# Performance work log

Measured on AMD Instinct MI355X. Metric: run time of the kernel, lower is better.

Reference implementation:

```python
import jax, jax.numpy as jnp
import numpy as np

BS = 128
E4M3_MAX = 448.0
E5M2_MAX = 57344.0


def qdq(x, fmax, dt):
    # block-wise (128-wide, last dim) fp8 quantize + dequantize (simulates act_quant + dequant in fp8_gemm)
    *lead, K = x.shape
    xb = x.reshape(*lead, K // BS, BS)
    s = jnp.maximum(jnp.max(jnp.abs(xb), axis=-1, keepdims=True) / fmax, 1e-12)
    xq = (xb / s).astype(dt).astype(jnp.float32)
    return (xq * s).reshape(*lead, K)


def fp8_linear(x, w, w_scale, fmax, dt, bias=None):
    # weight is fp8-valued (stored as f32 of the rounded values) with per-output-row-block scales
    x_dq = qdq(x, fmax, dt)
    sv = jnp.repeat(w_scale, BS)[: w.shape[0]]
    y = jnp.einsum('btk,ok->bto', x_dq, w * sv[:, None])
    return y if bias is None else y + bias


def fp8_ln(x, g, gs, b, bsc, eps=1e-5):
    mean = jnp.mean(x, axis=-1, keepdims=True)
    var = jnp.mean(jnp.square(x - mean), axis=-1, keepdims=True)  # unbiased=False
    xn = (x - mean) / jnp.sqrt(var + eps)
    d = x.shape[-1]
    return xn * (g * jnp.repeat(gs, BS)[:d]) + (b * jnp.repeat(bsc, BS)[:d])


def _fwd(x, attn_mask, wq, qs, wk, ks, wv, vs, wo, os_, fc1_w, fc1_s, fc1_b, fc2_w, fc2_s, fc2_b,
         ln1_g, ln1_gs, ln1_b, ln1_bs, ln2_g, ln2_gs, ln2_b, ln2_bs):
    B, T, C = x.shape
    H = 16
    HD = C // H
    e5 = jnp.float8_e5m2
    # attention (q/k/v/out projections use E5M2 fp8)
    q = fp8_linear(x, wq, qs, E5M2_MAX, e5).reshape(B, T, H, HD).transpose(0, 2, 1, 3)
    k = fp8_linear(x, wk, ks, E5M2_MAX, e5).reshape(B, T, H, HD).transpose(0, 2, 1, 3)
    v = fp8_linear(x, wv, vs, E5M2_MAX, e5).reshape(B, T, H, HD).transpose(0, 2, 1, 3)
    scores = jnp.einsum('bhqd,bhkd->bhqk', q, k) / jnp.sqrt(jnp.float32(HD))
    scores = jnp.where(attn_mask[:, None] == 0, -jnp.inf, scores)
    attn = jax.nn.softmax(scores, axis=-1)  # dropout = identity (eval)
    ctx = jnp.einsum('bhqk,bhkd->bhqd', attn, v).transpose(0, 2, 1, 3).reshape(B, T, C)
    attn_out = fp8_linear(ctx, wo, os_, E5M2_MAX, e5)
    x = fp8_ln(x + attn_out, ln1_g, ln1_gs, ln1_b, ln1_bs)
    # MLP (E4M3 fp8)
    e4 = jnp.float8_e4m3fn
    h = fp8_linear(x, fc1_w, fc1_s, E4M3_MAX, e4, fc1_b)
    h = jax.nn.gelu(h, approximate=False)  # torch nn.GELU default = exact erf
    ffn = fp8_linear(h, fc2_w, fc2_s, E4M3_MAX, e4, fc2_b)
    x = fp8_ln(x + ffn, ln2_g, ln2_gs, ln2_b, ln2_bs)
    return x


def _xavier_fp8(key, out_f, in_f, dt):
    bound = float(np.sqrt(6.0 / (in_f + out_f)))
    w = jax.random.uniform(key, (out_f, in_f), jnp.float32, -bound, bound)
    return w.astype(dt).astype(jnp.float32)  # simulate fp8 storage


def setup_inputs() -> dict:
    key = jax.random.key(0)
    kk = jax.random.split(key, 8)
    B, T, C, MLP = 2, 1024, 2048, 8192
    e5, e4 = jnp.float8_e5m2, jnp.float8_e4m3fn
    x = jax.random.normal(kk[0], (B, T, C), jnp.float32)
    attn_mask = jnp.broadcast_to(jnp.tril(jnp.ones((T, T), jnp.int32))[None], (B, T, T))
    nb = C // BS  # 16
    inp = {
        'x': x,
        'attn_mask': attn_mask,
        'wq': _xavier_fp8(kk[1], C, C, e5), 'qs': jnp.ones(nb, jnp.float32),
        'wk': _xavier_fp8(kk[2], C, C, e5), 'ks': jnp.ones(nb, jnp.float32),
        'wv': _xavier_fp8(kk[3], C, C, e5), 'vs': jnp.ones(nb, jnp.float32),
        'wo': _xavier_fp8(kk[4], C, C, e5), 'os_': jnp.ones(nb, jnp.float32),
        'fc1_w': _xavier_fp8(kk[5], MLP, C, e4), 'fc1_s': jnp.ones(MLP // BS, jnp.float32), 'fc1_b': jnp.zeros(MLP, jnp.float32),
        'fc2_w': _xavier_fp8(kk[6], C, MLP, e4), 'fc2_s': jnp.ones(nb, jnp.float32), 'fc2_b': jnp.zeros(C, jnp.float32),
        'ln1_g': jnp.ones(C, jnp.float32), 'ln1_gs': jnp.ones(nb, jnp.float32),
        'ln1_b': jnp.zeros(C, jnp.float32), 'ln1_bs': jnp.ones(nb, jnp.float32),
        'ln2_g': jnp.ones(C, jnp.float32), 'ln2_gs': jnp.ones(nb, jnp.float32),
        'ln2_b': jnp.zeros(C, jnp.float32), 'ln2_bs': jnp.ones(nb, jnp.float32),
    }
    return inp


def reference(x, attn_mask, wq, qs, wk, ks, wv, vs, wo, os_, fc1_w, fc1_s, fc1_b, fc2_w, fc2_s, fc2_b,
              ln1_g, ln1_gs, ln1_b, ln1_bs, ln2_g, ln2_gs, ln2_b, ln2_bs):
    return _fwd(x, attn_mask, wq, qs, wk, ks, wv, vs, wo, os_, fc1_w, fc1_s, fc1_b, fc2_w, fc2_s, fc2_b,
                ln1_g, ln1_gs, ln1_b, ln1_bs, ln2_g, ln2_gs, ln2_b, ln2_bs)
```

## Files before the change

kernel.cpp:

```cpp
#include <hip/hip_runtime.h>
#include <cstdint>


typedef __bf16 bf16x8 __attribute__((ext_vector_type(8)));
typedef unsigned short u16x8 __attribute__((ext_vector_type(8)));
typedef float f32x4 __attribute__((ext_vector_type(4)));
typedef float f32x16 __attribute__((ext_vector_type(16)));
typedef int i32x8 __attribute__((ext_vector_type(8)));
typedef unsigned short u16;

#if __has_builtin(__builtin_amdgcn_exp2f)
#define EXP2F(x) __builtin_amdgcn_exp2f(x)
#else
#define EXP2F(x) exp2f(x)
#endif

__device__ __forceinline__ void gl_lds16(const void* g, void* l) {
  __builtin_amdgcn_global_load_lds(
      (const __attribute__((address_space(1))) void*)g,
      (__attribute__((address_space(3))) void*)l, 16, 0, 0);
}

struct u4x2 { uint4 a, b; };
__device__ __forceinline__ i32x8 pack8(uint4 lo, uint4 hi) {
  u4x2 t{lo, hi};
  return __builtin_bit_cast(i32x8, t);
}

__device__ __forceinline__ u16 bf16_rne(float v) {
  uint32_t u = __float_as_uint(v);
  u += 0x7FFFu + ((u >> 16) & 1u);
  return (u16)(u >> 16);
}

__device__ __forceinline__ float fp8_round(float v, int mbits, float minnorm, float subq) {
  float av = fabsf(v);
  if (av < minnorm) {
    return rintf(v / subq) * subq;
  }
  uint32_t u = __float_as_uint(v);
  const int shift = 23 - mbits;
  const uint32_t mask = (1u << shift) - 1u;
  const uint32_t rem = u & mask;
  uint32_t base = u & ~mask;
  const uint32_t half = 1u << (shift - 1);
  if (rem > half || (rem == half && ((base >> shift) & 1u))) base += (1u << shift);
  return __uint_as_float(base);
}

__device__ __forceinline__ uint8_t fp8_encode(float v, int mbits, int bias) {
  uint32_t u = __float_as_uint(v);
  uint32_t sign = (u >> 31) << 7;
  if ((u & 0x7FFFFFFFu) == 0) return (uint8_t)sign;
  int e = (int)((u >> 23) & 255u) - 127;
  if (e >= 1 - bias) {
    uint32_t mant = (u >> (23 - mbits)) & ((1u << mbits) - 1u);
    return (uint8_t)(sign | ((uint32_t)(e + bias) << mbits) | mant);
  }
  float q = fabsf(v) * __uint_as_float((uint32_t)(127 + bias - 1 + mbits) << 23);
  return (uint8_t)(sign | (uint32_t)q);
}

__device__ __forceinline__ uint8_t q_e5(float v, float sc) {
  return fp8_encode(fp8_round(v / sc, 2, 6.103515625e-05f, 1.52587890625e-05f), 2, 15);
}
__device__ __forceinline__ uint8_t q_e4(float v, float sc) {
  return fp8_encode(fp8_round(v / sc, 3, 0.015625f, 0.001953125f), 3, 7);
}

__global__ __launch_bounds__(256) void qdq_kernel(
    const float* __restrict__ x, uint8_t* __restrict__ q, float* __restrict__ sT,
    int nblk, int kbshift, float fmax, float minnorm, float subq, int mbits, int bias) {
  const int wid = blockIdx.x * 4 + (threadIdx.x >> 6);
  if (wid >= nblk) return;
  const int lane = threadIdx.x & 63;
  const size_t base = (size_t)wid * 128 + (size_t)lane * 2;
  float2 v = *(const float2*)(x + base);
  float am = fmaxf(fabsf(v.x), fabsf(v.y));
#pragma unroll
  for (int m = 32; m >= 1; m >>= 1) am = fmaxf(am, __shfl_xor(am, m));
  const float sc = fmaxf(am / fmax, 1e-12f);
  const float q0 = fp8_round(v.x / sc, mbits, minnorm, subq);
  const float q1 = fp8_round(v.y / sc, mbits, minnorm, subq);
  uchar2 o;
  o.x = fp8_encode(q0, mbits, bias);
  o.y = fp8_encode(q1, mbits, bias);
  *(uchar2*)(q + base) = o;
  if (lane == 0) {
    const int kbs = 1 << kbshift;
    const int m = wid >> kbshift;
    const int kb = wid & (kbs - 1);
    sT[(size_t)kb * (nblk >> kbshift) + m] = sc;
  }
}

__global__ __launch_bounds__(256) void w_to_fp8_kernel(
    const float* __restrict__ in, uint8_t* __restrict__ out, int n4, int mbits, int bias) {
  const int i = blockIdx.x * 256 + threadIdx.x;
  if (i >= n4) return;
  float4 v = ((const float4*)in)[i];
  uchar4 o;
  o.x = fp8_encode(v.x, mbits, bias);
  o.y = fp8_encode(v.y, mbits, bias);
  o.z = fp8_encode(v.z, mbits, bias);
  o.w = fp8_encode(v.w, mbits, bias);
  *(uchar4*)(out + (size_t)i * 4) = o;
}

__global__ __launch_bounds__(256) void w3_to_fp8_kernel(
    const float* __restrict__ a, const float* __restrict__ b,
    const float* __restrict__ c, uint8_t* __restrict__ out, int n4) {
  const int i = blockIdx.x * 256 + threadIdx.x;
  if (i >= n4) return;
  const float* in = blockIdx.y == 0 ? a : (blockIdx.y == 1 ? b : c);
  float4 v = ((const float4*)in)[i];
  uchar4 o;
  o.x = fp8_encode(v.x, 2, 15);
  o.y = fp8_encode(v.y, 2, 15);
  o.z = fp8_encode(v.z, 2, 15);
  o.w = fp8_encode(v.w, 2, 15);
  *(uchar4*)(out + (size_t)blockIdx.y * n4 * 4 + (size_t)i * 4) = o;
}

__global__ void concat3_kernel(const float* __restrict__ a, const float* __restrict__ b,
                               const float* __restrict__ c, float* __restrict__ o, int n) {
  const int i = threadIdx.x;
  if (i < n) { o[i] = a[i]; o[n + i] = b[i]; o[2 * n + i] = c[i]; }
}

__global__ __launch_bounds__(256) void split_bf16_kernel(
    const float* __restrict__ in, u16* __restrict__ hi, u16* __restrict__ lo, int n4) {
  const int i = blockIdx.x * 256 + threadIdx.x;
  if (i >= n4) return;
  float4 v = ((const float4*)in)[i];
  float f[4] = {v.x, v.y, v.z, v.w};
  ushort4 oh, ol;
  u16* ph = (u16*)&oh;
  u16* pl = (u16*)&ol;
#pragma unroll
  for (int j = 0; j < 4; ++j) {
    u16 h = bf16_rne(f[j]);
    float hf = __uint_as_float((uint32_t)h << 16);
    ph[j] = h;
    pl[j] = bf16_rne(f[j] - hf);
  }
  ((ushort4*)hi)[i] = oh;
  ((ushort4*)lo)[i] = ol;
}

__global__ __launch_bounds__(256) void vtrans_kernel(
    const float* __restrict__ v, u16* __restrict__ vth, u16* __restrict__ vtl) {
  __shared__ float tile[64][65];
  const int tid = threadIdx.x;
  const int t0 = blockIdx.x * 64;
  const int d0 = blockIdx.y * 64;
  const int bh = blockIdx.z;
  const int b = bh >> 4, h = bh & 15;
#pragma unroll
  for (int s = 0; s < 4; ++s) {
    const int e = s * 256 + tid;
    const int r = e >> 4, c4 = e & 15;
    float4 val = *(const float4*)(v + ((size_t)(b * 1024 + t0 + r)) * 2048 + h * 128 + d0 + c4 * 4);
    tile[r][c4 * 4 + 0] = val.x;
    tile[r][c4 * 4 + 1] = val.y;
    tile[r][c4 * 4 + 2] = val.z;
    tile[r][c4 * 4 + 3] = val.w;
  }
  __syncthreads();
#pragma unroll
  for (int s = 0; s < 4; ++s) {
    const int e = s * 256 + tid;
    const int dr = e >> 4, tc4 = e & 15;
    ushort4 oh, ol;
    u16* ph = (u16*)&oh;
    u16* pl = (u16*)&ol;
#pragma unroll
    for (int i = 0; i < 4; ++i) {
      float f = tile[tc4 * 4 + i][dr];
      u16 hv = bf16_rne(f);
      ph[i] = hv;
      pl[i] = bf16_rne(f - __uint_as_float((uint32_t)hv << 16));
    }
    const size_t ob = ((size_t)(bh * 128 + d0 + dr)) * 1024 + t0 + tc4 * 4;
    *(ushort4*)(vth + ob) = oh;
    *(ushort4*)(vtl + ob) = ol;
  }
}

__global__ __launch_bounds__(256, 2) void attn_wave_kernel(
    const float* __restrict__ Q, const u16* __restrict__ Kh, const u16* __restrict__ Kl,
    const u16* __restrict__ Vth, const u16* __restrict__ Vtl,
    uint8_t* __restrict__ Aqo, float* __restrict__ sTo) {
  constexpr int PLD = 34;
  __shared__ uint32_t Psm[4][32 * PLD];
  __shared__ float Osum[32 * 128];
  __shared__ float lsh[4][32];

  const int tid = threadIdx.x;
  const int w = tid >> 6;
  const int lane = tid & 63;
  const int l31 = lane & 31;
  const int q2 = lane >> 5;
  const int bh = blockIdx.x;
  const int b = bh >> 4;
  const int hofs = (bh & 15) * 128;
  const int qt = 31 - (int)blockIdx.y;
  const int i0 = qt * 32;
  const float SC2 = 0.12752698f;

  bf16x8 qh[8], ql[8];
  {
    const float* qp = Q + ((size_t)(b * 1024 + i0 + l31)) * 2048 + hofs + q2 * 8;
#pragma unroll
    for (int c = 0; c < 8; ++c) {
      float4 v0 = *(const float4*)(qp + c * 16);
      float4 v1 = *(const float4*)(qp + c * 16 + 4);
      float f[8] = {v0.x, v0.y, v0.z, v0.w, v1.x, v1.y, v1.z, v1.w};
      u16x8 uh, ul;
#pragma unroll
      for (int j = 0; j < 8; ++j) {
        u16 hv = bf16_rne(f[j]);
        uh[j] = hv;
        ul[j] = bf16_rne(f[j] - __uint_as_float((uint32_t)hv << 16));
      }
      qh[c] = __builtin_bit_cast(bf16x8, uh);
      ql[c] = __builtin_bit_cast(bf16x8, ul);
    }
  }

  const f32x16 z16 = {0.f};
  f32x16 Oacc[4] = {z16, z16, z16, z16};
  float lr[16];
#pragma unroll
  for (int r = 0; r < 16; ++r) lr[r] = 0.f;
  int rowq[16];
#pragma unroll
  for (int r = 0; r < 16; ++r) rowq[r] = (r & 3) + 8 * (r >> 2) + 4 * q2;

  uint32_t* Pw = Psm[w];
  for (int kt = w; kt <= qt; kt += 4) {
    const int j0 = kt * 32;
    const size_t krow = ((size_t)(b * 1024 + j0 + l31)) * 2048 + hofs + q2 * 8;
    f32x16 S = z16;
#pragma unroll
    for (int c = 0; c < 8; ++c) {
      bf16x8 k8h = *(const bf16x8*)(Kh + krow + c * 16);
      bf16x8 k8l = *(const bf16x8*)(Kl + krow + c * 16);
      __builtin_amdgcn_s_setprio(1);
      S = __builtin_amdgcn_mfma_f32_32x32x16_bf16(qh[c], k8h, S, 0, 0, 0);
      S = __builtin_amdgcn_mfma_f32_32x32x16_bf16(qh[c], k8l, S, 0, 0, 0);
      S = __builtin_amdgcn_mfma_f32_32x32x16_bf16(ql[c], k8h, S, 0, 0, 0);
      __builtin_amdgcn_s_setprio(0);
    }
    if (kt == qt) {
#pragma unroll
      for (int r = 0; r < 16; ++r)
        if (l31 > rowq[r]) S[r] = -3e38f;
    }
#pragma unroll
    for (int r = 0; r < 16; ++r) {
      const float p = EXP2F(S[r] * SC2);
      lr[r] += p;
      const u16 ph = bf16_rne(p);
      const u16 pl = bf16_rne(p - __uint_as_float((uint32_t)ph << 16));
      Pw[rowq[r] * PLD + l31] = (uint32_t)ph | ((uint32_t)pl << 16);
    }
#pragma unroll
    for (int s = 0; s < 2; ++s) {
      const uint32_t* rp = Pw + l31 * PLD + s * 16 + q2 * 8;
      uint2 a0 = *(const uint2*)(rp + 0);
      uint2 a1 = *(const uint2*)(rp + 2);
      uint2 a2 = *(const uint2*)(rp + 4);
      uint2 a3 = *(const uint2*)(rp + 6);
      u16x8 uh, ul;
      uh[0] = (u16)a0.x; ul[0] = (u16)(a0.x >> 16);
      uh[1] = (u16)a0.y; ul[1] = (u16)(a0.y >> 16);
      uh[2] = (u16)a1.x; ul[2] = (u16)(a1.x >> 16);
      uh[3] = (u16)a1.y; ul[3] = (u16)(a1.y >> 16);
      uh[4] = (u16)a2.x; ul[4] = (u16)(a2.x >> 16);
      uh[5] = (u16)a2.y; ul[5] = (u16)(a2.y >> 16);
      uh[6] = (u16)a3.x; ul[6] = (u16)(a3.x >> 16);
      uh[7] = (u16)a3.y; ul[7] = (u16)(a3.y >> 16);
      bf16x8 p8h = __builtin_bit_cast(bf16x8, uh);
      bf16x8 p8l = __builtin_bit_cast(bf16x8, ul);
      const size_t vrow = ((size_t)(bh * 128 + l31)) * 1024 + j0 + s * 16 + q2 * 8;
#pragma unroll
      for (int dt = 0; dt < 4; ++dt) {
        bf16x8 v8h = *(const bf16x8*)(Vth + vrow + (size_t)dt * 32768);
        bf16x8 v8l = *(const bf16x8*)(Vtl + vrow + (size_t)dt * 32768);
        __builtin_amdgcn_s_setprio(1);
        Oacc[dt] = __builtin_amdgcn_mfma_f32_32x32x16_bf16(p8h, v8h, Oacc[dt], 0, 0, 0);
        Oacc[dt] = __builtin_amdgcn_mfma_f32_32x32x16_bf16(p8h, v8l, Oacc[dt], 0, 0, 0);
        Oacc[dt] = __builtin_amdgcn_mfma_f32_32x32x16_bf16(p8l, v8h, Oacc[dt], 0, 0, 0);
        __builtin_amdgcn_s_setprio(0);
      }
    }
  }

#pragma unroll
  for (int r = 0; r < 16; ++r) {
    float t = lr[r];
    t += __shfl_xor(t, 1);
    t += __shfl_xor(t, 2);
    t += __shfl_xor(t, 4);
    t += __shfl_xor(t, 8);
    t += __shfl_xor(t, 16);
    lr[r] = t;
  }
  if (l31 == 0) {
#pragma unroll
    for (int r = 0; r < 16; ++r) lsh[w][rowq[r]] = lr[r];
  }
  if (w == 0) {
#pragma unroll
    for (int dt = 0; dt < 4; ++dt)
#pragma unroll
      for (int r = 0; r < 16; ++r) Osum[rowq[r] * 128 + dt * 32 + l31] = Oacc[dt][r];
  }
  __syncthreads();
  if (w == 1) {
#pragma unroll
    for (int dt = 0; dt < 4; ++dt)
#pragma unroll
      for (int r = 0; r < 16; ++r) Osum[rowq[r] * 128 + dt * 32 + l31] += Oacc[dt][r];
  }
  __syncthreads();
  if (w == 2) {
#pragma unroll
    for (int dt = 0; dt < 4; ++dt)
#pragma unroll
      for (int r = 0; r < 16; ++r) Osum[rowq[r] * 128 + dt * 32 + l31] += Oacc[dt][r];
  }
  __syncthreads();
  if (w == 3) {
#pragma unroll
    for (int dt = 0; dt < 4; ++dt)
#pragma unroll
      for (int r = 0; r < 16; ++r) Osum[rowq[r] * 128 + dt * 32 + l31] += Oacc[dt][r];
  }
  __syncthreads();
  const int row = w * 8 + (lane >> 3);
  const int c0 = (lane & 7) * 16;
  const float inv = 1.0f / (lsh[0][row] + lsh[1][row] + lsh[2][row] + lsh[3][row]);
  float vq[16];
  float am = 0.f;
#pragma unroll
  for (int i2 = 0; i2 < 4; ++i2) {
    float4 v = *(const float4*)(Osum + row * 128 + c0 + i2 * 4);
    vq[i2 * 4 + 0] = v.x * inv;
    vq[i2 * 4 + 1] = v.y * inv;
    vq[i2 * 4 + 2] = v.z * inv;
    vq[i2 * 4 + 3] = v.w * inv;
  }
#pragma unroll
  for (int t = 0; t < 16; ++t) am = fmaxf(am, fabsf(vq[t]));
  am = fmaxf(am, __shfl_xor(am, 1));
  am = fmaxf(am, __shfl_xor(am, 2));
  am = fmaxf(am, __shfl_xor(am, 4));
  const float sc = fmaxf(am / 57344.f, 1e-12f);
  uint8_t qb8[16];
#pragma unroll
  for (int t = 0; t < 16; ++t) qb8[t] = q_e5(vq[t], sc);
  const int token = b * 1024 + i0 + row;
  *(uint4*)(Aqo + (size_t)token * 2048 + hofs + c0) = *(const uint4*)qb8;
  if ((lane & 7) == 0) sTo[(size_t)(bh & 15) * 2048 + token] = sc;
}

template <int FMT, int QOUT>
__global__ __launch_bounds__(256, 2) void gemm_simple(
    const uint8_t* __restrict__ A, const float* __restrict__ sxT,
    const uint8_t* __restrict__ W, const float* __restrict__ wsc,
    const float* __restrict__ bias, float* __restrict__ out,
    uint8_t* __restrict__ outq, float* __restrict__ sTq,
    int M, int N, int K, int gelu, int seg_shift, int Nw) {
  __shared__ uint8_t As[128 * 128];
  __shared__ uint8_t Ws[128 * 128];
  __shared__ float rowred[2][128];
  const int tid = threadIdx.x;
  const int lane = tid & 63;
  const int wave = tid >> 6;
  const int wm = (wave >> 1) * 64;
  const int wn = (wave & 1) * 64;
  const int l31 = lane & 31;
  const int q2 = lane >> 5;
  const int bm = blockIdx.y * 128;
  const int bn = blockIdx.x * 128;

  const int srow = wave * 8 + (lane >> 3);
  const int gchunk = (lane & 7) ^ (lane >> 3);
  const uint8_t* ga = A + (size_t)(bm + srow) * K + gchunk * 16;
  const uint8_t* gw = W + (size_t)(bn + srow) * K + gchunk * 16;
  uint8_t* la = As + srow * 128 + (lane & 7) * 16;
  uint8_t* lw = Ws + srow * 128 + (lane & 7) * 16;

  const f32x16 z16 = {0.f};
  f32x16 acc[2][2] = {{z16, z16}, {z16, z16}};

  const int nk = K >> 7;
  for (int kt = 0; kt < nk; ++kt) {
    __syncthreads();
#pragma unroll
    for (int s = 0; s < 4; ++s) {
      gl_lds16(ga + (size_t)s * 32 * K, la + s * 4096);
      gl_lds16(gw + (size_t)s * 32 * K, lw + s * 4096);
    }
    ga += 128;
    gw += 128;
    __syncthreads();
    f32x16 chk[2][2] = {{z16, z16}, {z16, z16}};
#pragma unroll
    for (int mf = 0; mf < 2; ++mf) {
      i32x8 af[2], bf2[2];
      const int c = mf * 4 + q2 * 2;
#pragma unroll
      for (int i = 0; i < 2; ++i) {
        const int r = wm + i * 32 + l31;
        const uint8_t* Ar = As + r * 128;
        const int s7 = r & 7;
        af[i] = pack8(*(const uint4*)(Ar + ((c ^ s7) * 16)),
                      *(const uint4*)(Ar + (((c + 1) ^ s7) * 16)));
      }
#pragma unroll
      for (int j = 0; j < 2; ++j) {
        const int r = wn + j * 32 + l31;
        const uint8_t* Wr = Ws + r * 128;
        const int s7 = r & 7;
        bf2[j] = pack8(*(const uint4*)(Wr + ((c ^ s7) * 16)),
                       *(const uint4*)(Wr + (((c + 1) ^ s7) * 16)));
      }
#pragma unroll
      for (int i = 0; i < 2; ++i)
#pragma unroll
        for (int j = 0; j < 2; ++j)
          chk[i][j] = __builtin_amdgcn_mfma_scale_f32_32x32x64_f8f6f4(
              af[i], bf2[j], chk[i][j], FMT, FMT, 0, 0x7F7F7F7F, 0, 0x7F7F7F7F);
    }
#pragma unroll
    for (int i = 0; i < 2; ++i) {
#pragma unroll
      for (int rg = 0; rg < 4; ++rg) {
        const f32x4 sv = *(const f32x4*)(sxT + (size_t)kt * M + bm + wm + i * 32 + rg * 8 + q2 * 4);
#pragma unroll
        for (int j = 0; j < 2; ++j)
#pragma unroll
          for (int rr = 0; rr < 4; ++rr)
            acc[i][j][rg * 4 + rr] += sv[rr] * chk[i][j][rg * 4 + rr];
      }
    }
  }

  if (QOUT) {
#pragma unroll
    for (int i = 0; i < 2; ++i) {
#pragma unroll
      for (int j = 0; j < 2; ++j) {
        const int n = bn + wn + j * 32 + l31;
        const float wsn = wsc[n >> 7];
        const float bv = bias[n];
#pragma unroll
        for (int reg = 0; reg < 16; ++reg) {
          float v = acc[i][j][reg] * wsn + bv;
          acc[i][j][reg] = 0.5f * v * (1.f + erff(v * 0.70710678118654752440f));
        }
      }
    }
#pragma unroll
    for (int i = 0; i < 2; ++i) {
      float am2[16];
#pragma unroll
      for (int reg = 0; reg < 16; ++reg)
        am2[reg] = fmaxf(fabsf(acc[i][0][reg]), fabsf(acc[i][1][reg]));
#pragma unroll
      for (int reg = 0; reg < 16; ++reg) {
        am2[reg] = fmaxf(am2[reg], __shfl_xor(am2[reg], 1));
        am2[reg] = fmaxf(am2[reg], __shfl_xor(am2[reg], 2));
        am2[reg] = fmaxf(am2[reg], __shfl_xor(am2[reg], 4));
        am2[reg] = fmaxf(am2[reg], __shfl_xor(am2[reg], 8));
        am2[reg] = fmaxf(am2[reg], __shfl_xor(am2[reg], 16));
      }
      if (l31 == 0) {
#pragma unroll
        for (int reg = 0; reg < 16; ++reg)
          rowred[wave & 1][wm + i * 32 + (reg & 3) + 8 * (reg >> 2) + 4 * q2] = am2[reg];
      }
    }
    __syncthreads();
#pragma unroll
    for (int i = 0; i < 2; ++i) {
#pragma unroll
      for (int reg = 0; reg < 16; ++reg) {
        const int rloc = wm + i * 32 + (reg & 3) + 8 * (reg >> 2) + 4 * q2;
        const float sc = fmaxf(fmaxf(rowred[0][rloc], rowred[1][rloc]) / 448.f, 1e-12f);
        const int m = bm + rloc;
#pragma unroll
        for (int j = 0; j < 2; ++j)
          outq[(size_t)m * N + bn + wn + j * 32 + l31] = q_e4(acc[i][j][reg], sc);
        if ((wave & 1) == 0 && l31 == 0) sTq[(size_t)(bn >> 7) * M + m] = sc;
      }
    }
    return;
  }

#pragma unroll
  for (int i = 0; i < 2; ++i) {
#pragma unroll
    for (int j = 0; j < 2; ++j) {
      const int n = bn + wn + j * 32 + l31;
      const float wsn = wsc[n >> 7];
      const float bv = bias ? bias[n] : 0.f;
      const int seg = n >> seg_shift;
      const int col = n & ((1 << seg_shift) - 1);
      float* op = out + (size_t)seg * M * Nw + col;
#pragma unroll
      for (int reg = 0; reg < 16; ++reg) {
        const int m = bm + wm + i * 32 + (reg & 3) + 8 * (reg >> 2) + 4 * q2;
        float v = acc[i][j][reg] * wsn + bv;
        if (gelu) v = 0.5f * v * (1.f + erff(v * 0.70710678118654752440f));
        op[(size_t)m * Nw] = v;
      }
    }
  }
}

template <int QOUT>
__global__ __launch_bounds__(256) void ln_kernel(
    const float* __restrict__ a, const float* __restrict__ b2,
    const float* __restrict__ g, const float* __restrict__ gs,
    const float* __restrict__ bb, const float* __restrict__ bs,
    float* __restrict__ out, uint8_t* __restrict__ outq, float* __restrict__ sT,
    int C) {
  __shared__ float red[4];
  __shared__ float wred[8][4];
  const int tid = threadIdx.x;
  const int row = blockIdx.x;
  const float* pa = a + (size_t)row * C;
  const float* pb = b2 + (size_t)row * C;
  float v[8];
  float sum = 0.f;
#pragma unroll
  for (int k = 0; k < 8; ++k) {
    const int c = tid + (k << 8);
    v[k] = pa[c] + pb[c];
    sum += v[k];
  }
#pragma unroll
  for (int m = 32; m >= 1; m >>= 1) sum += __shfl_xor(sum, m);
  if ((tid & 63) == 0) red[tid >> 6] = sum;
  __syncthreads();
  const float mean = (red[0] + red[1] + red[2] + red[3]) * (1.f / 2048.f);
  __syncthreads();
  float sq = 0.f;
#pragma unroll
  for (int k = 0; k < 8; ++k) {
    const float d = v[k] - mean;
    sq += d * d;
  }
#pragma unroll
  for (int m = 32; m >= 1; m >>= 1) sq += __shfl_xor(sq, m);
  if ((tid & 63) == 0) red[tid >> 6] = sq;
  __syncthreads();
  const float var = (red[0] + red[1] + red[2] + red[3]) * (1.f / 2048.f);
  const float inv = 1.0f / sqrtf(var + 1e-5f);
  float* po = out + (size_t)row * C;
  float o[8];
#pragma unroll
  for (int k = 0; k < 8; ++k) {
    const int c = tid + (k << 8);
    o[k] = (v[k] - mean) * inv * (g[c] * gs[c >> 7]) + bb[c] * bs[c >> 7];
    po[c] = o[k];
  }
  if (QOUT) {
    const int w = tid >> 6;
#pragma unroll
    for (int k = 0; k < 8; ++k) {
      float am = fabsf(o[k]);
      am = fmaxf(am, __shfl_xor(am, 1));
      am = fmaxf(am, __shfl_xor(am, 2));
      am = fmaxf(am, __shfl_xor(am, 4));
      am = fmaxf(am, __shfl_xor(am, 8));
      am = fmaxf(am, __shfl_xor(am, 16));
      am = fmaxf(am, __shfl_xor(am, 32));
      if ((tid & 63) == 0) wred[k][w] = am;
    }
    __syncthreads();
    const int hsel = (tid >> 7) * 2;
#pragma unroll
    for (int k = 0; k < 8; ++k) {
      const float bm = fmaxf(wred[k][hsel], wred[k][hsel + 1]);
      const float sc = fmaxf(bm / 448.f, 1e-12f);
      const int c = tid + (k << 8);
      outq[(size_t)row * C + c] = q_e4(o[k], sc);
      if ((tid & 127) == 0) sT[(size_t)((k << 1) | (tid >> 7)) * 2048 + row] = sc;
    }
  }
}

extern "C" void kernel_launch(void* const* d_in, const int* in_sizes, int n_in,
                              void* d_out, int out_size, void* d_ws, size_t ws_size,
                              hipStream_t stream) {
  const int C = 2048, MLP = 8192;
  const int M = 2048;

  const float* x = (const float*)d_in[0];
  const float* wq = (const float*)d_in[2];
  const float* qs = (const float*)d_in[3];
  const float* wk = (const float*)d_in[4];
  const float* ks = (const float*)d_in[5];
  const float* wv = (const float*)d_in[6];
  const float* vs = (const float*)d_in[7];
  const float* wo = (const float*)d_in[8];
  const float* os_ = (const float*)d_in[9];
  const float* fc1_w = (const float*)d_in[10];
  const float* fc1_s = (const float*)d_in[11];
  const float* fc1_b = (const float*)d_in[12];
  const float* fc2_w = (const float*)d_in[13];
  const float* fc2_s = (const float*)d_in[14];
  const float* fc2_b = (const float*)d_in[15];
  const float* ln1_g = (const float*)d_in[16];
  const float* ln1_gs = (const float*)d_in[17];
  const float* ln1_b = (const float*)d_in[18];
  const float* ln1_bs = (const float*)d_in[19];
  const float* ln2_g = (const float*)d_in[20];
  const float* ln2_gs = (const float*)d_in[21];
  const float* ln2_b = (const float*)d_in[22];
  const float* ln2_bs = (const float*)d_in[23];

  char* ws = (char*)d_ws;
  const size_t o_Aq = 0;
  const size_t o_Wb = 33554432;
  const size_t o_sx = 67108864;
  const size_t o_ln1 = 67633152;
  const size_t o_q = 84410368;
  const size_t o_k = 101187584;
  const size_t o_v = 117964800;
  const size_t o_ctx = 134742016;
  const size_t o_attn = 151519232;
  const size_t o_ffn = o_attn;
  if (ws_size < 168296448ull) return;

  uint8_t* Aq = (uint8_t*)(ws + o_Aq);
  uint8_t* Wb = (uint8_t*)(ws + o_Wb);
  float* sx = (float*)(ws + o_sx);
  float* wsc3 = (float*)(ws + o_sx + 262144);
  float* ln1o = (float*)(ws + o_ln1);
  float* qb = (float*)(ws + o_q);
  float* kb = (float*)(ws + o_k);
  float* vb = (float*)(ws + o_v);
  uint8_t* Aq2 = (uint8_t*)(ws + o_ctx);
  float* attn_out = (float*)(ws + o_attn);
  uint8_t* Aq3 = (uint8_t*)(ws + o_q);
  float* sxk = (float*)(ws + o_k);
  float* ffn = (float*)(ws + o_ffn);
  float* outp = (float*)d_out;
  u16* Kh = (u16*)(ws + o_Aq);
  u16* Kl = (u16*)(ws + o_Aq + 8388608);
  u16* Vth = (u16*)(ws + o_Aq + 16777216);
  u16* Vtl = (u16*)(ws + o_Aq + 25165824);

  const float E5_MAX = 57344.f, E5_MINN = 6.103515625e-05f, E5_SUBQ = 1.52587890625e-05f;
  const float E4_MAX = 448.f, E4_MINN = 0.015625f, E4_SUBQ = 0.001953125f;

  const dim3 blk(256);
  const int wc_qkv = (C * C / 4 + 255) / 256;
  const int wc_fc = (C * MLP / 4 + 255) / 256;

  qdq_kernel<<<M * (C / 128) / 4, blk, 0, stream>>>(x, Aq, sx, M * (C / 128), 4, E5_MAX, E5_MINN, E5_SUBQ, 2, 15);
  w3_to_fp8_kernel<<<dim3(wc_qkv, 3), blk, 0, stream>>>(wq, wk, wv, Wb, C * C / 4);
  concat3_kernel<<<1, 64, 0, stream>>>(qs, ks, vs, wsc3, C / 128);
  gemm_simple<1, 0><<<dim3(3 * C / 128, M / 128), blk, 0, stream>>>(
      Aq, sx, Wb, wsc3, nullptr, qb, nullptr, nullptr, M, 3 * C, C, 0, 11, C);

  split_bf16_kernel<<<(M * C / 4 + 255) / 256, blk, 0, stream>>>(kb, Kh, Kl, M * C / 4);
  vtrans_kernel<<<dim3(16, 2, 32), blk, 0, stream>>>(vb, Vth, Vtl);
  attn_wave_kernel<<<dim3(32, 32), blk, 0, stream>>>(qb, Kh, Kl, Vth, Vtl, Aq2, sx);

  w_to_fp8_kernel<<<wc_qkv, blk, 0, stream>>>(wo, Wb, C * C / 4, 2, 15);
  gemm_simple<1, 0><<<dim3(C / 128, M / 128), blk, 0, stream>>>(
      Aq2, sx, Wb, os_, nullptr, attn_out, nullptr, nullptr, M, C, C, 0, 30, C);

  ln_kernel<1><<<M, blk, 0, stream>>>(x, attn_out, ln1_g, ln1_gs, ln1_b, ln1_bs,
                                      ln1o, Aq, sx, C);

  w_to_fp8_kernel<<<wc_fc, blk, 0, stream>>>(fc1_w, Wb, C * MLP / 4, 3, 7);
  gemm_simple<0, 1><<<dim3(MLP / 128, M / 128), blk, 0, stream>>>(
      Aq, sx, Wb, fc1_s, fc1_b, nullptr, Aq3, sxk, M, MLP, C, 1, 30, MLP);

  w_to_fp8_kernel<<<wc_fc, blk, 0, stream>>>(fc2_w, Wb, C * MLP / 4, 3, 7);
  gemm_simple<0, 0><<<dim3(C / 128, M / 128), blk, 0, stream>>>(
      Aq3, sxk, Wb, fc2_s, fc2_b, ffn, nullptr, nullptr, M, C, MLP, 0, 30, C);

  ln_kernel<0><<<M, blk, 0, stream>>>(ln1o, ffn, ln2_g, ln2_gs, ln2_b, ln2_bs,
                                      outp, nullptr, nullptr, C);
}
```

Before: 657.2 us.

## Fuse QKV bf16 hi/lo split and V transpose into the QKV GEMM epilogue

The QKV GEMM epilogue now writes Q, K and V directly as bf16 hi/lo pairs, staging through shared memory to transpose V into the head-dim-major layout. This removes the separate split_bf16 and vtrans kernels and the fp32 Q/K/V round trip through global memory. The attention kernel now loads precomputed bf16 Q halves instead of converting fp32 Q itself. The cost is a heavier GEMM epilogue with two extra barrier phases and reuse of the GEMM's shared tile memory as the transpose buffer.

```diff
diff --git a/kernel.cpp b/kernel.cpp
--- a/kernel.cpp
+++ b/kernel.cpp
@@ -128,67 +128,9 @@
   if (i < n) { o[i] = a[i]; o[n + i] = b[i]; o[2 * n + i] = c[i]; }
 }
 
-__global__ __launch_bounds__(256) void split_bf16_kernel(
-    const float* __restrict__ in, u16* __restrict__ hi, u16* __restrict__ lo, int n4) {
-  const int i = blockIdx.x * 256 + threadIdx.x;
-  if (i >= n4) return;
-  float4 v = ((const float4*)in)[i];
-  float f[4] = {v.x, v.y, v.z, v.w};
-  ushort4 oh, ol;
-  u16* ph = (u16*)&oh;
-  u16* pl = (u16*)&ol;
-#pragma unroll
-  for (int j = 0; j < 4; ++j) {
-    u16 h = bf16_rne(f[j]);
-    float hf = __uint_as_float((uint32_t)h << 16);
-    ph[j] = h;
-    pl[j] = bf16_rne(f[j] - hf);
-  }
-  ((ushort4*)hi)[i] = oh;
-  ((ushort4*)lo)[i] = ol;
-}
-
-__global__ __launch_bounds__(256) void vtrans_kernel(
-    const float* __restrict__ v, u16* __restrict__ vth, u16* __restrict__ vtl) {
-  __shared__ float tile[64][65];
-  const int tid = threadIdx.x;
-  const int t0 = blockIdx.x * 64;
-  const int d0 = blockIdx.y * 64;
-  const int bh = blockIdx.z;
-  const int b = bh >> 4, h = bh & 15;
-#pragma unroll
-  for (int s = 0; s < 4; ++s) {
-    const int e = s * 256 + tid;
-    const int r = e >> 4, c4 = e & 15;
-    float4 val = *(const float4*)(v + ((size_t)(b * 1024 + t0 + r)) * 2048 + h * 128 + d0 + c4 * 4);
-    tile[r][c4 * 4 + 0] = val.x;
-    tile[r][c4 * 4 + 1] = val.y;
-    tile[r][c4 * 4 + 2] = val.z;
-    tile[r][c4 * 4 + 3] = val.w;
-  }
-  __syncthreads();
-#pragma unroll
-  for (int s = 0; s < 4; ++s) {
-    const int e = s * 256 + tid;
-    const int dr = e >> 4, tc4 = e & 15;
-    ushort4 oh, ol;
-    u16* ph = (u16*)&oh;
-    u16* pl = (u16*)&ol;
-#pragma unroll
-    for (int i = 0; i < 4; ++i) {
-      float f = tile[tc4 * 4 + i][dr];
-      u16 hv = bf16_rne(f);
-      ph[i] = hv;
-      pl[i] = bf16_rne(f - __uint_as_float((uint32_t)hv << 16));
-    }
-    const size_t ob = ((size_t)(bh * 128 + d0 + dr)) * 1024 + t0 + tc4 * 4;
-    *(ushort4*)(vth + ob) = oh;
-    *(ushort4*)(vtl + ob) = ol;
-  }
-}
-
 __global__ __launch_bounds__(256, 2) void attn_wave_kernel(
-    const float* __restrict__ Q, const u16* __restrict__ Kh, const u16* __restrict__ Kl,
+    const u16* __restrict__ Qh, const u16* __restrict__ Ql,
+    const u16* __restrict__ Kh, const u16* __restrict__ Kl,
     const u16* __restrict__ Vth, const u16* __restrict__ Vtl,
     uint8_t* __restrict__ Aqo, float* __restrict__ sTo) {
   constexpr int PLD = 34;
@@ -210,21 +152,11 @@
 
   bf16x8 qh[8], ql[8];
   {
-    const float* qp = Q + ((size_t)(b * 1024 + i0 + l31)) * 2048 + hofs + q2 * 8;
+    const size_t qrow = ((size_t)(b * 1024 + i0 + l31)) * 2048 + hofs + q2 * 8;
 #pragma unroll
     for (int c = 0; c < 8; ++c) {
-      float4 v0 = *(const float4*)(qp + c * 16);
-      float4 v1 = *(const float4*)(qp + c * 16 + 4);
-      float f[8] = {v0.x, v0.y, v0.z, v0.w, v1.x, v1.y, v1.z, v1.w};
-      u16x8 uh, ul;
-#pragma unroll
-      for (int j = 0; j < 8; ++j) {
-        u16 hv = bf16_rne(f[j]);
-        uh[j] = hv;
-        ul[j] = bf16_rne(f[j] - __uint_as_float((uint32_t)hv << 16));
-      }
-      qh[c] = __builtin_bit_cast(bf16x8, uh);
-      ql[c] = __builtin_bit_cast(bf16x8, ul);
+      qh[c] = *(const bf16x8*)(Qh + qrow + c * 16);
+      ql[c] = *(const bf16x8*)(Ql + qrow + c * 16);
     }
   }
 
@@ -366,16 +298,22 @@
   if ((lane & 7) == 0) sTo[(size_t)(bh & 15) * 2048 + token] = sc;
 }
 
-template <int FMT, int QOUT>
+template <int FMT, int EPI>
 __global__ __launch_bounds__(256, 2) void gemm_simple(
     const uint8_t* __restrict__ A, const float* __restrict__ sxT,
     const uint8_t* __restrict__ W, const float* __restrict__ wsc,
     const float* __restrict__ bias, float* __restrict__ out,
     uint8_t* __restrict__ outq, float* __restrict__ sTq,
+    u16* __restrict__ Qh, u16* __restrict__ Ql,
+    u16* __restrict__ Kh, u16* __restrict__ Kl,
+    u16* __restrict__ Vth, u16* __restrict__ Vtl,
     int M, int N, int K, int gelu, int seg_shift, int Nw) {
-  __shared__ uint8_t As[128 * 128];
-  __shared__ uint8_t Ws[128 * 128];
-  __shared__ float rowred[2][128];
+  __shared__ uint8_t smem[33792];
+  uint8_t* As = smem;
+  uint8_t* Ws = smem + 16384;
+  float* rowred = (float*)(smem + 32768);
+  uint32_t(*tsm)[66] = (uint32_t(*)[66])smem;
+
   const int tid = threadIdx.x;
   const int lane = tid & 63;
   const int wave = tid >> 6;
@@ -449,7 +387,73 @@
     }
   }
 
-  if (QOUT) {
+  if (EPI == 2) {
+    const int seg = bn >> 11;
+    const int col0 = bn & 2047;
+    const int b = bm >> 10;
+    const int t0g = bm & 1023;
+    const int h = col0 >> 7;
+#pragma unroll
+    for (int p = 0; p < 2; ++p) {
+      __syncthreads();
+      if ((wave & 1) == p) {
+#pragma unroll
+        for (int i = 0; i < 2; ++i)
+#pragma unroll
+          for (int j = 0; j < 2; ++j) {
+            const int n = bn + wn + j * 32 + l31;
+            const float wsn = wsc[n >> 7];
+            const int dloc = j * 32 + l31;
+#pragma unroll
+            for (int reg = 0; reg < 16; ++reg) {
+              const int tl = wm + i * 32 + (reg & 3) + 8 * (reg >> 2) + 4 * q2;
+              const float v = acc[i][j][reg] * wsn;
+              const u16 hv = bf16_rne(v);
+              const u16 lv = bf16_rne(v - __uint_as_float((uint32_t)hv << 16));
+              tsm[tl][dloc] = (uint32_t)hv | ((uint32_t)lv << 16);
+            }
+          }
+      }
+      __syncthreads();
+      u16 hbuf[32], lbuf[32];
+      if (seg < 2) {
+        u16* OH = seg == 0 ? Qh : Kh;
+        u16* OL = seg == 0 ? Ql : Kl;
+        const int row = tid >> 1;
+        const int cb = (tid & 1) * 32;
+#pragma unroll
+        for (int c = 0; c < 32; ++c) {
+          const uint32_t pk = tsm[row][cb + c];
+          hbuf[c] = (u16)pk;
+          lbuf[c] = (u16)(pk >> 16);
+        }
+        const size_t ob = (size_t)(bm + row) * 2048 + col0 + p * 64 + cb;
+#pragma unroll
+        for (int c = 0; c < 4; ++c) {
+          *(uint4*)(OH + ob + c * 8) = *(const uint4*)(hbuf + c * 8);
+          *(uint4*)(OL + ob + c * 8) = *(const uint4*)(lbuf + c * 8);
+        }
+      } else {
+        const int d = p * 64 + (tid >> 2);
+        const int toff = (tid & 3) * 32;
+#pragma unroll
+        for (int c = 0; c < 32; ++c) {
+          const uint32_t pk = tsm[toff + c][tid >> 2];
+          hbuf[c] = (u16)pk;
+          lbuf[c] = (u16)(pk >> 16);
+        }
+        const size_t ob = ((size_t)((b * 16 + h) * 128 + d)) * 1024 + t0g + toff;
+#pragma unroll
+        for (int c = 0; c < 4; ++c) {
+          *(uint4*)(Vth + ob + c * 8) = *(const uint4*)(hbuf + c * 8);
+          *(uint4*)(Vtl + ob + c * 8) = *(const uint4*)(lbuf + c * 8);
+        }
+      }
+    }
+    return;
+  }
+
+  if (EPI == 1) {
 #pragma unroll
     for (int i = 0; i < 2; ++i) {
 #pragma unroll
@@ -481,7 +485,7 @@
       if (l31 == 0) {
 #pragma unroll
         for (int reg = 0; reg < 16; ++reg)
-          rowred[wave & 1][wm + i * 32 + (reg & 3) + 8 * (reg >> 2) + 4 * q2] = am2[reg];
+          rowred[(wave & 1) * 128 + wm + i * 32 + (reg & 3) + 8 * (reg >> 2) + 4 * q2] = am2[reg];
       }
     }
     __syncthreads();
@@ -490,7 +494,7 @@
 #pragma unroll
       for (int reg = 0; reg < 16; ++reg) {
         const int rloc = wm + i * 32 + (reg & 3) + 8 * (reg >> 2) + 4 * q2;
-        const float sc = fmaxf(fmaxf(rowred[0][rloc], rowred[1][rloc]) / 448.f, 1e-12f);
+        const float sc = fmaxf(fmaxf(rowred[rloc], rowred[128 + rloc]) / 448.f, 1e-12f);
         const int m = bm + rloc;
 #pragma unroll
         for (int j = 0; j < 2; ++j)
@@ -643,22 +647,20 @@
   float* sx = (float*)(ws + o_sx);
   float* wsc3 = (float*)(ws + o_sx + 262144);
   float* ln1o = (float*)(ws + o_ln1);
-  float* qb = (float*)(ws + o_q);
-  float* kb = (float*)(ws + o_k);
-  float* vb = (float*)(ws + o_v);
+  u16* Qh = (u16*)(ws + o_q);
+  u16* Ql = (u16*)(ws + o_q + 8388608);
+  u16* Kh = (u16*)(ws + o_k);
+  u16* Kl = (u16*)(ws + o_k + 8388608);
+  u16* Vth = (u16*)(ws + o_v);
+  u16* Vtl = (u16*)(ws + o_v + 8388608);
   uint8_t* Aq2 = (uint8_t*)(ws + o_ctx);
   float* attn_out = (float*)(ws + o_attn);
   uint8_t* Aq3 = (uint8_t*)(ws + o_q);
   float* sxk = (float*)(ws + o_k);
   float* ffn = (float*)(ws + o_ffn);
   float* outp = (float*)d_out;
-  u16* Kh = (u16*)(ws + o_Aq);
-  u16* Kl = (u16*)(ws + o_Aq + 8388608);
-  u16* Vth = (u16*)(ws + o_Aq + 16777216);
-  u16* Vtl = (u16*)(ws + o_Aq + 25165824);
 
   const float E5_MAX = 57344.f, E5_MINN = 6.103515625e-05f, E5_SUBQ = 1.52587890625e-05f;
-  const float E4_MAX = 448.f, E4_MINN = 0.015625f, E4_SUBQ = 0.001953125f;
 
   const dim3 blk(256);
   const int wc_qkv = (C * C / 4 + 255) / 256;
@@ -667,27 +669,29 @@
   qdq_kernel<<<M * (C / 128) / 4, blk, 0, stream>>>(x, Aq, sx, M * (C / 128), 4, E5_MAX, E5_MINN, E5_SUBQ, 2, 15);
   w3_to_fp8_kernel<<<dim3(wc_qkv, 3), blk, 0, stream>>>(wq, wk, wv, Wb, C * C / 4);
   concat3_kernel<<<1, 64, 0, stream>>>(qs, ks, vs, wsc3, C / 128);
-  gemm_simple<1, 0><<<dim3(3 * C / 128, M / 128), blk, 0, stream>>>(
-      Aq, sx, Wb, wsc3, nullptr, qb, nullptr, nullptr, M, 3 * C, C, 0, 11, C);
-
-  split_bf16_kernel<<<(M * C / 4 + 255) / 256, blk, 0, stream>>>(kb, Kh, Kl, M * C / 4);
-  vtrans_kernel<<<dim3(16, 2, 32), blk, 0, stream>>>(vb, Vth, Vtl);
-  attn_wave_kernel<<<dim3(32, 32), blk, 0, stream>>>(qb, Kh, Kl, Vth, Vtl, Aq2, sx);
+  gemm_simple<1, 2><<<dim3(3 * C / 128, M / 128), blk, 0, stream>>>(
+      Aq, sx, Wb, wsc3, nullptr, nullptr, nullptr, nullptr,
+      Qh, Ql, Kh, Kl, Vth, Vtl, M, 3 * C, C, 0, 11, C);
+
+  attn_wave_kernel<<<dim3(32, 32), blk, 0, stream>>>(Qh, Ql, Kh, Kl, Vth, Vtl, Aq2, sx);
 
   w_to_fp8_kernel<<<wc_qkv, blk, 0, stream>>>(wo, Wb, C * C / 4, 2, 15);
   gemm_simple<1, 0><<<dim3(C / 128, M / 128), blk, 0, stream>>>(
-      Aq2, sx, Wb, os_, nullptr, attn_out, nullptr, nullptr, M, C, C, 0, 30, C);
+      Aq2, sx, Wb, os_, nullptr, attn_out, nullptr, nullptr,
+      nullptr, nullptr, nullptr, nullptr, nullptr, nullptr, M, C, C, 0, 30, C);
 
   ln_kernel<1><<<M, blk, 0, stream>>>(x, attn_out, ln1_g, ln1_gs, ln1_b, ln1_bs,
                                       ln1o, Aq, sx, C);
 
   w_to_fp8_kernel<<<wc_fc, blk, 0, stream>>>(fc1_w, Wb, C * MLP / 4, 3, 7);
   gemm_simple<0, 1><<<dim3(MLP / 128, M / 128), blk, 0, stream>>>(
-      Aq, sx, Wb, fc1_s, fc1_b, nullptr, Aq3, sxk, M, MLP, C, 1, 30, MLP);
+      Aq, sx, Wb, fc1_s, fc1_b, nullptr, Aq3, sxk,
+      nullptr, nullptr, nullptr, nullptr, nullptr, nullptr, M, MLP, C, 1, 30, MLP);
 
   w_to_fp8_kernel<<<wc_fc, blk, 0, stream>>>(fc2_w, Wb, C * MLP / 4, 3, 7);
   gemm_simple<0, 0><<<dim3(C / 128, M / 128), blk, 0, stream>>>(
-      Aq3, sxk, Wb, fc2_s, fc2_b, ffn, nullptr, nullptr, M, C, MLP, 0, 30, C);
+      Aq3, sxk, Wb, fc2_s, fc2_b, ffn, nullptr, nullptr,
+      nullptr, nullptr, nullptr, nullptr, nullptr, nullptr, M, C, MLP, 0, 30, C);
 
   ln_kernel<0><<<M, blk, 0, stream>>>(ln1o, ffn, ln2_g, ln2_gs, ln2_b, ln2_bs,
                                       outp, nullptr, nullptr, C);
```

After: 655.1 us. Within noise of the previous version (-0.3%).
